# Performance work log

Hardware: AMD Instinct MI355X
Metric: run time of the kernel (lower is better)

The kernel has to match this reference:

```python
import jax, jax.numpy as jnp
import numpy as np

NPOINT = 1024
RADIUS = 0.2
NSAMPLE = 32


def fps(xyz, npoint):
    """Furthest point sampling. xyz: (B, N, 3) -> idx (B, npoint) int32.
    Sequential farthest-distance selection, first point is index 0 (matches CUDA kernel)."""
    def one(pts):
        N = pts.shape[0]
        def step(carry, _):
            dists, last = carry
            d = jnp.sum((pts - pts[last]) ** 2, axis=-1)   # (N,)
            dists = jnp.minimum(dists, d)
            nxt = jnp.argmax(dists).astype(jnp.int32)
            return (dists, nxt), last
        init = (jnp.full((N,), 1e10, dtype=pts.dtype), jnp.int32(0))
        _, idx = jax.lax.scan(step, init, None, length=npoint)
        return idx
    return jax.vmap(one)(xyz)


def ball_query(xyz, new_xyz, radius, nsample):
    """For each centroid, indices of first nsample points within radius;
    slots with no hit are filled with the first hit (centroid itself is always a hit)."""
    N = xyz.shape[1]
    d2 = jnp.sum((new_xyz[:, :, None, :] - xyz[:, None, :, :]) ** 2, axis=-1)  # (B, npoint, N)
    cand = jnp.where(d2 < radius * radius, jnp.arange(N, dtype=jnp.int32), jnp.int32(N))
    neg_topk, _ = jax.lax.top_k(-cand, nsample)  # smallest nsample candidate indices
    idx = -neg_topk                               # ascending order, misses == N
    first = idx[..., :1]
    return jnp.where(idx == N, first, idx)


_batched_gather = jax.vmap(lambda a, i: a[i])  # a: (N, C), i: (...,) -> (..., C)


def reference(xyz, normal, features, w1, b1, w2, b2, w3, b3):
    # --- FPS sampling + gather of centroids ---
    fps_idx = fps(xyz, NPOINT)                          # (B, npoint)
    new_xyz = _batched_gather(xyz, fps_idx)             # (B, npoint, 3)
    new_normal = _batched_gather(normal, fps_idx)       # (B, npoint, 3)

    # --- ball-query grouping ---
    idx = ball_query(xyz, new_xyz, RADIUS, NSAMPLE)     # (B, npoint, nsample)
    grouped_xyz = _batched_gather(xyz, idx) - new_xyz[:, :, None, :]  # relative coords
    grouped_feat = _batched_gather(features, idx)        # (B, npoint, nsample, C)
    h = jnp.concatenate([grouped_xyz, grouped_feat], axis=-1)  # (B, npoint, nsample, 3+C)

    # --- shared per-neighborhood MLP (1x1 convs) + max pool over neighbors ---
    h = jax.nn.relu(jnp.einsum('bpsc,co->bpso', h, w1) + b1)
    h = jax.nn.relu(jnp.einsum('bpsc,co->bpso', h, w2) + b2)
    h = jax.nn.relu(jnp.einsum('bpsc,co->bpso', h, w3) + b3)
    new_features = jnp.max(h, axis=2)                   # (B, npoint, 128)
    new_features = jnp.transpose(new_features, (0, 2, 1))  # (B, 128, npoint) channel-first
    return new_xyz, new_normal, new_features


def setup_inputs() -> dict:
    key = jax.random.key(0)
    ks = jax.random.split(key, 9)
    B, N, C = 8, 8192, 32
    cin = 3 + C
    return {
        'xyz': jax.random.uniform(ks[0], (B, N, 3), dtype=jnp.float32),
        'normal': jax.random.normal(ks[1], (B, N, 3), dtype=jnp.float32),
        'features': jax.random.normal(ks[2], (B, N, C), dtype=jnp.float32),
        'w1': jax.random.normal(ks[3], (cin, 64), dtype=jnp.float32) * (1.0 / np.sqrt(cin)),
        'b1': jnp.zeros((64,), dtype=jnp.float32),
        'w2': jax.random.normal(ks[4], (64, 64), dtype=jnp.float32) * (1.0 / np.sqrt(64)),
        'b2': jnp.zeros((64,), dtype=jnp.float32),
        'w3': jax.random.normal(ks[5], (64, 128), dtype=jnp.float32) * (1.0 / np.sqrt(64)),
        'b3': jnp.zeros((128,), dtype=jnp.float32),
    }
```

## Files before the change

### kernel.cpp

```cpp
#include <hip/hip_runtime.h>

#define NB 8
#define NN 8192
#define NC 32
#define NPOINT 1024
#define NSAMPLE 32

__device__ __forceinline__ float d2_exact(float ax, float ay, float az,
                                          float bx, float by, float bz) {
    float dx = __fsub_rn(ax, bx);
    float dy = __fsub_rn(ay, by);
    float dz = __fsub_rn(az, bz);
    return __fadd_rn(__fadd_rn(__fmul_rn(dx, dx), __fmul_rn(dy, dy)),
                     __fmul_rn(dz, dz));
}

#define FPS_T 256
#define FPS_K (NN / FPS_T)
#define NCONS 248
#define NBLK (NB + NCONS)
#define K2_WAVES 4
#define SLOTS_PER_PASS (NCONS * K2_WAVES)
#define NPASS ((NB * NPOINT + SLOTS_PER_PASS - 1) / SLOTS_PER_PASS)

#define XS 37
#define HS 65

#define SMEM_BYTES 102464

__device__ __forceinline__ unsigned long long kmax64(unsigned long long a,
                                                     unsigned long long b) {
    double r = fmax(__longlong_as_double((long long)a),
                    __longlong_as_double((long long)b));
    return (unsigned long long)__double_as_longlong(r);
}

template <int CTRL, int RM>
__device__ __forceinline__ unsigned long long dpp_k(unsigned long long k) {
    unsigned hi = (unsigned)__builtin_amdgcn_update_dpp(
        0, (int)(k >> 32), CTRL, RM, 0xf, true);
    unsigned lo = (unsigned)__builtin_amdgcn_update_dpp(
        0, (int)(k & 0xffffffffULL), CTRL, RM, 0xf, true);
    return ((unsigned long long)hi << 32) | lo;
}

__device__ __forceinline__ void barrier_lds_only() {
    asm volatile("s_waitcnt lgkmcnt(0)\n\ts_barrier" ::: "memory");
}

__global__ __launch_bounds__(256, 1) void fused_kernel(
    const float* __restrict__ xyz, const float* __restrict__ normal,
    const float* __restrict__ features,
    const float* __restrict__ w1, const float* __restrict__ b1,
    const float* __restrict__ w2, const float* __restrict__ b2,
    const float* __restrict__ w3, const float* __restrict__ b3,
    float* __restrict__ out_xyz, float* __restrict__ out_normal,
    float* __restrict__ out_feat, int* __restrict__ idxbuf) {

    __shared__ __align__(16) char smem[SMEM_BYTES];

    if (blockIdx.x < NB) {
        unsigned long long (*redk)[4] = (unsigned long long (*)[4])(smem);
        int*   sel_hist = (int*)(smem + 64);
        float* sxyz     = (float*)(smem + 64 + 4096);

        const int b = blockIdx.x;
        const float* bx = xyz + (size_t)b * NN * 3;
        const int tid = threadIdx.x;
        const int lane = tid & 63;
        const int wave = tid >> 6;
        int* idxg = idxbuf + (b << 10);

        float px[FPS_K], py[FPS_K], pz[FPS_K], dist[FPS_K];
#pragma unroll
        for (int k = 0; k < FPS_K; ++k) {
            int p = tid + k * FPS_T;
            float x = bx[p * 3 + 0];
            float y = bx[p * 3 + 1];
            float z = bx[p * 3 + 2];
            px[k] = x; py[k] = y; pz[k] = z;
            sxyz[p * 3 + 0] = x;
            sxyz[p * 3 + 1] = y;
            sxyz[p * 3 + 2] = z;
            dist[k] = 1e10f;
        }
#pragma unroll
        for (int k = 0; k < FPS_K; ++k) {
            asm volatile("" : "+v"(px[k]), "+v"(py[k]), "+v"(pz[k]));
        }

        int cur = 0;
        float lx = bx[0], ly = bx[1], lz = bx[2];

        for (int it = 0; it < NPOINT; ++it) {
            const int par = it & 1;
            if (tid == 0) sel_hist[it] = cur;

            float bv[4] = {-1.0f, -1.0f, -1.0f, -1.0f};
            int bk[4] = {0, 0, 0, 0};
#pragma unroll
            for (int k = 0; k < FPS_K; ++k) {
                const int c = k >> 3;
                float d = d2_exact(px[k], py[k], pz[k], lx, ly, lz);
                float nd = fminf(dist[k], d);
                dist[k] = nd;
                bool gt = nd > bv[c];
                bv[c] = gt ? nd : bv[c];
                bk[c] = gt ? k : bk[c];
            }
            bool g1 = bv[1] > bv[0];
            float v01 = g1 ? bv[1] : bv[0];
            int   k01 = g1 ? bk[1] : bk[0];
            bool g3 = bv[3] > bv[2];
            float v23 = g3 ? bv[3] : bv[2];
            int   k23 = g3 ? bk[3] : bk[2];
            bool gf = v23 > v01;
            float bvf = gf ? v23 : v01;
            int   bkf = gf ? k23 : k01;

            int bp = tid + (bkf << 8);
            unsigned long long key =
                ((unsigned long long)__float_as_uint(bvf) << 32) |
                (unsigned)(~bp);

            key = kmax64(key, dpp_k<0x111, 0xf>(key));
            key = kmax64(key, dpp_k<0x112, 0xf>(key));
            key = kmax64(key, dpp_k<0x114, 0xf>(key));
            key = kmax64(key, dpp_k<0x118, 0xf>(key));
            key = kmax64(key, dpp_k<0x142, 0xa>(key));
            key = kmax64(key, dpp_k<0x143, 0xc>(key));
            if (lane == 63) redk[par][wave] = key;
            barrier_lds_only();

            unsigned long long g =
                kmax64(kmax64(redk[par][0], redk[par][1]),
                       kmax64(redk[par][2], redk[par][3]));
            int p = (int)(~(unsigned)(g & 0xffffffffULL));
            p = __builtin_amdgcn_readfirstlane(p);
            lx = sxyz[p * 3 + 0];
            ly = sxyz[p * 3 + 1];
            lz = sxyz[p * 3 + 2];
            cur = p;

            if (((it & 15) == 15) && tid < 16) {
                int t = (it & ~15) + tid;
                __hip_atomic_store(idxg + t, sel_hist[t], __ATOMIC_RELAXED,
                                   __HIP_MEMORY_SCOPE_AGENT);
            }
        }
        __syncthreads();

        const float* bn = normal + (size_t)b * NN * 3;
        for (int t = tid; t < NPOINT; t += FPS_T) {
            int i = sel_hist[t];
            size_t o = ((size_t)b * NPOINT + t) * 3;
            out_xyz[o + 0] = sxyz[i * 3 + 0];
            out_xyz[o + 1] = sxyz[i * 3 + 1];
            out_xyz[o + 2] = sxyz[i * 3 + 2];
            out_normal[o + 0] = bn[i * 3 + 0];
            out_normal[o + 1] = bn[i * 3 + 1];
            out_normal[o + 2] = bn[i * 3 + 2];
        }
    } else {
        int*   sel_all  = (int*)smem;
        float* bufA_all = (float*)(smem + 512);
        float* bufB_all = (float*)(smem + 33792);

        const int cb = blockIdx.x - NB;
        const int wave = threadIdx.x >> 6;
        const int lane = threadIdx.x & 63;
        int*   sel = sel_all + wave * 32;
        float* XA  = bufA_all + wave * 2080;
        float* XB  = bufB_all + wave * 2080;

        for (int pass = 0; pass < NPASS; ++pass) {
            int k = pass * SLOTS_PER_PASS + (cb * K2_WAVES + wave);
            if (k >= NB * NPOINT) k -= NB * NPOINT;
            const int b = k & 7;
            const int t = k >> 3;
            const int g = (b << 10) + t;
            const int p = t;
            const float* bxp = xyz + (size_t)b * NN * 3;
            const float* bfp = features + (size_t)b * NN * NC;

            int v = __hip_atomic_load(idxbuf + g, __ATOMIC_RELAXED,
                                      __HIP_MEMORY_SCOPE_AGENT);
            while (v < 0) {
                __builtin_amdgcn_s_sleep(8);
                v = __hip_atomic_load(idxbuf + g, __ATOMIC_RELAXED,
                                      __HIP_MEMORY_SCOPE_AGENT);
            }
            const float cx = bxp[v * 3 + 0];
            const float cy = bxp[v * 3 + 1];
            const float cz = bxp[v * 3 + 2];

            int have = 0;
            for (int ch = 0; ch < NN / 64 && have < NSAMPLE; ++ch) {
                int j = ch * 64 + lane;
                float x = bxp[j * 3 + 0], y = bxp[j * 3 + 1], z = bxp[j * 3 + 2];
                float d2 = d2_exact(x, y, z, cx, cy, cz);
                bool hit = d2 < 0.04f;
                unsigned long long m = __ballot(hit);
                int pos = have + __popcll(m & ((1ull << lane) - 1ull));
                if (hit && pos < NSAMPLE) sel[pos] = j;
                have += __popcll(m);
            }
            __syncthreads();
            int nsel = have < NSAMPLE ? have : NSAMPLE;
            int first = sel[0];
            if (lane < NSAMPLE && lane >= nsel) sel[lane] = first;
            __syncthreads();

            {
                int s = lane >> 1, h = lane & 1;
                int row = sel[s];
                const float* fr = bfp + (size_t)row * NC + h * 16;
#pragma unroll
                for (int q = 0; q < 4; ++q) {
                    float4 vv = *(const float4*)(fr + q * 4);
                    int base = s * XS + 3 + h * 16 + q * 4;
                    XA[base + 0] = vv.x; XA[base + 1] = vv.y;
                    XA[base + 2] = vv.z; XA[base + 3] = vv.w;
                }
                if (h == 0) {
                    XA[s * XS + 0] = __fsub_rn(bxp[row * 3 + 0], cx);
                    XA[s * XS + 1] = __fsub_rn(bxp[row * 3 + 1], cy);
                    XA[s * XS + 2] = __fsub_rn(bxp[row * 3 + 2], cz);
                }
            }
            __syncthreads();

            const int sg = lane >> 3;
            const int og = lane & 7;

            {
                float acc[4][8];
#pragma unroll
                for (int j = 0; j < 4; ++j)
#pragma unroll
                    for (int o = 0; o < 8; ++o) acc[j][o] = 0.f;
                for (int c = 0; c < 35; ++c) {
                    float xv[4];
#pragma unroll
                    for (int j = 0; j < 4; ++j) xv[j] = XA[(sg * 4 + j) * XS + c];
                    const float* wr = w1 + c * 64 + og * 8;
                    float4 wa = *(const float4*)(wr);
                    float4 wb = *(const float4*)(wr + 4);
                    float w8[8] = {wa.x, wa.y, wa.z, wa.w, wb.x, wb.y, wb.z, wb.w};
#pragma unroll
                    for (int j = 0; j < 4; ++j)
#pragma unroll
                        for (int o = 0; o < 8; ++o) acc[j][o] += xv[j] * w8[o];
                }
                float4 ba = *(const float4*)(b1 + og * 8);
                float4 bb = *(const float4*)(b1 + og * 8 + 4);
                float bias[8] = {ba.x, ba.y, ba.z, ba.w, bb.x, bb.y, bb.z, bb.w};
#pragma unroll
                for (int j = 0; j < 4; ++j)
#pragma unroll
                    for (int o = 0; o < 8; ++o)
                        XB[(sg * 4 + j) * HS + og * 8 + o] =
                            fmaxf(acc[j][o] + bias[o], 0.f);
            }
            __syncthreads();

            {
                float acc[4][8];
#pragma unroll
                for (int j = 0; j < 4; ++j)
#pragma unroll
                    for (int o = 0; o < 8; ++o) acc[j][o] = 0.f;
                for (int c = 0; c < 64; ++c) {
                    float xv[4];
#pragma unroll
                    for (int j = 0; j < 4; ++j) xv[j] = XB[(sg * 4 + j) * HS + c];
                    const float* wr = w2 + c * 64 + og * 8;
                    float4 wa = *(const float4*)(wr);
                    float4 wb = *(const float4*)(wr + 4);
                    float w8[8] = {wa.x, wa.y, wa.z, wa.w, wb.x, wb.y, wb.z, wb.w};
#pragma unroll
                    for (int j = 0; j < 4; ++j)
#pragma unroll
                        for (int o = 0; o < 8; ++o) acc[j][o] += xv[j] * w8[o];
                }
                float4 ba = *(const float4*)(b2 + og * 8);
                float4 bb = *(const float4*)(b2 + og * 8 + 4);
                float bias[8] = {ba.x, ba.y, ba.z, ba.w, bb.x, bb.y, bb.z, bb.w};
#pragma unroll
                for (int j = 0; j < 4; ++j)
#pragma unroll
                    for (int o = 0; o < 8; ++o)
                        XA[(sg * 4 + j) * HS + og * 8 + o] =
                            fmaxf(acc[j][o] + bias[o], 0.f);
            }
            __syncthreads();

            {
                float acc[4][16];
#pragma unroll
                for (int j = 0; j < 4; ++j)
#pragma unroll
                    for (int o = 0; o < 16; ++o) acc[j][o] = 0.f;
                for (int c = 0; c < 64; ++c) {
                    float xv[4];
#pragma unroll
                    for (int j = 0; j < 4; ++j) xv[j] = XA[(sg * 4 + j) * HS + c];
                    const float* wr = w3 + c * 128 + og * 16;
                    float4 wq[4];
#pragma unroll
                    for (int q = 0; q < 4; ++q) wq[q] = *(const float4*)(wr + q * 4);
                    float w16[16] = {wq[0].x, wq[0].y, wq[0].z, wq[0].w,
                                     wq[1].x, wq[1].y, wq[1].z, wq[1].w,
                                     wq[2].x, wq[2].y, wq[2].z, wq[2].w,
                                     wq[3].x, wq[3].y, wq[3].z, wq[3].w};
#pragma unroll
                    for (int j = 0; j < 4; ++j)
#pragma unroll
                        for (int o = 0; o < 16; ++o) acc[j][o] += xv[j] * w16[o];
                }
                float m[16];
#pragma unroll
                for (int o = 0; o < 16; ++o) {
                    float t0 = fmaxf(acc[0][o], acc[1][o]);
                    float t1 = fmaxf(acc[2][o], acc[3][o]);
                    m[o] = fmaxf(t0, t1);
                }
#pragma unroll
                for (int off = 8; off <= 32; off <<= 1)
#pragma unroll
                    for (int o = 0; o < 16; ++o)
                        m[o] = fmaxf(m[o], __shfl_xor(m[o], off));
                if (sg == 0) {
                    float4 bq[4];
#pragma unroll
                    for (int q = 0; q < 4; ++q)
                        bq[q] = *(const float4*)(b3 + og * 16 + q * 4);
                    float bias[16] = {bq[0].x, bq[0].y, bq[0].z, bq[0].w,
                                      bq[1].x, bq[1].y, bq[1].z, bq[1].w,
                                      bq[2].x, bq[2].y, bq[2].z, bq[2].w,
                                      bq[3].x, bq[3].y, bq[3].z, bq[3].w};
#pragma unroll
                    for (int o = 0; o < 16; ++o) {
                        float val = fmaxf(m[o] + bias[o], 0.f);
                        out_feat[((size_t)b * 128 + og * 16 + o) * NPOINT + p] = val;
                    }
                }
            }
        }
    }
}

extern "C" void kernel_launch(void* const* d_in, const int* in_sizes, int n_in,
                              void* d_out, int out_size, void* d_ws, size_t ws_size,
                              hipStream_t stream) {
    const float* xyz      = (const float*)d_in[0];
    const float* normal   = (const float*)d_in[1];
    const float* features = (const float*)d_in[2];
    const float* w1 = (const float*)d_in[3];
    const float* b1 = (const float*)d_in[4];
    const float* w2 = (const float*)d_in[5];
    const float* b2 = (const float*)d_in[6];
    const float* w3 = (const float*)d_in[7];
    const float* b3 = (const float*)d_in[8];

    float* out        = (float*)d_out;
    float* out_xyz    = out;
    float* out_normal = out + NB * NPOINT * 3;
    float* out_feat   = out + 2 * NB * NPOINT * 3;
    int*   idxbuf     = (int*)d_ws;

    hipMemsetAsync(idxbuf, 0xFF, NB * NPOINT * sizeof(int), stream);

    hipLaunchKernelGGL(fused_kernel, dim3(NBLK), dim3(256), 0, stream,
                       xyz, normal, features, w1, b1, w2, b2, w3, b3,
                       out_xyz, out_normal, out_feat, idxbuf);
}
```

Baseline: 1.025 ms.

## Pack FPS distance math into v_pk ops and split wave argmax reduction

Stores the FPS point coordinates as float2 pairs and computes the squared distances with packed v_pk_add/v_pk_mul instructions, halving the VALU instruction count for the distance update. The 64-bit key DPP reduction is replaced by a float max reduction, a readlane, and then an unsigned min reduction over the indices of lanes holding the max, so the ties rule stays the same. Selected indices are now published to global memory one per iteration by thread 0 rather than in batches of 16, so consumer blocks see them earlier at the cost of a global store each iteration. Packed add of the negated centroid plus separate mul and add should match the original rounding, though this depends on v_pk ops not fusing.

After: 1.127 ms. 10.0% more time.

```diff
diff --git a/kernel.cpp b/kernel.cpp
--- a/kernel.cpp
+++ b/kernel.cpp
@@ -28,6 +28,19 @@
 
 #define SMEM_BYTES 102464
 
+typedef float f32x2 __attribute__((ext_vector_type(2)));
+
+__device__ __forceinline__ f32x2 pk_add(f32x2 a, f32x2 b) {
+    f32x2 d;
+    asm("v_pk_add_f32 %0, %1, %2" : "=v"(d) : "v"(a), "v"(b));
+    return d;
+}
+__device__ __forceinline__ f32x2 pk_mul(f32x2 a, f32x2 b) {
+    f32x2 d;
+    asm("v_pk_mul_f32 %0, %1, %2" : "=v"(d) : "v"(a), "v"(b));
+    return d;
+}
+
 __device__ __forceinline__ unsigned long long kmax64(unsigned long long a,
                                                      unsigned long long b) {
     double r = fmax(__longlong_as_double((long long)a),
@@ -36,12 +49,14 @@
 }
 
 template <int CTRL, int RM>
-__device__ __forceinline__ unsigned long long dpp_k(unsigned long long k) {
-    unsigned hi = (unsigned)__builtin_amdgcn_update_dpp(
-        0, (int)(k >> 32), CTRL, RM, 0xf, true);
-    unsigned lo = (unsigned)__builtin_amdgcn_update_dpp(
-        0, (int)(k & 0xffffffffULL), CTRL, RM, 0xf, true);
-    return ((unsigned long long)hi << 32) | lo;
+__device__ __forceinline__ float dpp_f(float x) {
+    return __int_as_float(__builtin_amdgcn_update_dpp(
+        0, __float_as_int(x), CTRL, RM, 0xf, true));
+}
+template <int CTRL, int RM>
+__device__ __forceinline__ unsigned dpp_u(unsigned x) {
+    return (unsigned)__builtin_amdgcn_update_dpp(
+        -1, (int)x, CTRL, RM, 0xf, false);
 }
 
 __device__ __forceinline__ void barrier_lds_only() {
@@ -71,22 +86,24 @@
         const int wave = tid >> 6;
         int* idxg = idxbuf + (b << 10);
 
-        float px[FPS_K], py[FPS_K], pz[FPS_K], dist[FPS_K];
+        f32x2 px[FPS_K / 2], py[FPS_K / 2], pz[FPS_K / 2];
+        float dist[FPS_K];
 #pragma unroll
         for (int k = 0; k < FPS_K; ++k) {
             int p = tid + k * FPS_T;
             float x = bx[p * 3 + 0];
             float y = bx[p * 3 + 1];
             float z = bx[p * 3 + 2];
-            px[k] = x; py[k] = y; pz[k] = z;
             sxyz[p * 3 + 0] = x;
             sxyz[p * 3 + 1] = y;
             sxyz[p * 3 + 2] = z;
+            if ((k & 1) == 0) { px[k >> 1].x = x; py[k >> 1].x = y; pz[k >> 1].x = z; }
+            else              { px[k >> 1].y = x; py[k >> 1].y = y; pz[k >> 1].y = z; }
             dist[k] = 1e10f;
         }
 #pragma unroll
-        for (int k = 0; k < FPS_K; ++k) {
-            asm volatile("" : "+v"(px[k]), "+v"(py[k]), "+v"(pz[k]));
+        for (int q = 0; q < FPS_K / 2; ++q) {
+            asm volatile("" : "+v"(px[q]), "+v"(py[q]), "+v"(pz[q]));
         }
 
         int cur = 0;
@@ -94,19 +111,36 @@
 
         for (int it = 0; it < NPOINT; ++it) {
             const int par = it & 1;
-            if (tid == 0) sel_hist[it] = cur;
+            if (tid == 0) {
+                sel_hist[it] = cur;
+                __hip_atomic_store(idxg + it, cur, __ATOMIC_RELAXED,
+                                   __HIP_MEMORY_SCOPE_AGENT);
+            }
+
+            f32x2 nlx = {-lx, -lx};
+            f32x2 nly = {-ly, -ly};
+            f32x2 nlz = {-lz, -lz};
 
             float bv[4] = {-1.0f, -1.0f, -1.0f, -1.0f};
             int bk[4] = {0, 0, 0, 0};
 #pragma unroll
-            for (int k = 0; k < FPS_K; ++k) {
-                const int c = k >> 3;
-                float d = d2_exact(px[k], py[k], pz[k], lx, ly, lz);
-                float nd = fminf(dist[k], d);
-                dist[k] = nd;
-                bool gt = nd > bv[c];
-                bv[c] = gt ? nd : bv[c];
-                bk[c] = gt ? k : bk[c];
+            for (int q = 0; q < FPS_K / 2; ++q) {
+                const int c = q >> 2;
+                f32x2 dx = pk_add(px[q], nlx);
+                f32x2 dy = pk_add(py[q], nly);
+                f32x2 dz = pk_add(pz[q], nlz);
+                f32x2 d2 = pk_add(pk_add(pk_mul(dx, dx), pk_mul(dy, dy)),
+                                  pk_mul(dz, dz));
+                float nd0 = fminf(dist[2 * q + 0], d2.x);
+                float nd1 = fminf(dist[2 * q + 1], d2.y);
+                dist[2 * q + 0] = nd0;
+                dist[2 * q + 1] = nd1;
+                bool g0 = nd0 > bv[c];
+                bv[c] = g0 ? nd0 : bv[c];
+                bk[c] = g0 ? 2 * q + 0 : bk[c];
+                bool g1 = nd1 > bv[c];
+                bv[c] = g1 ? nd1 : bv[c];
+                bk[c] = g1 ? 2 * q + 1 : bk[c];
             }
             bool g1 = bv[1] > bv[0];
             float v01 = g1 ? bv[1] : bv[0];
@@ -119,17 +153,31 @@
             int   bkf = gf ? k23 : k01;
 
             int bp = tid + (bkf << 8);
-            unsigned long long key =
-                ((unsigned long long)__float_as_uint(bvf) << 32) |
-                (unsigned)(~bp);
-
-            key = kmax64(key, dpp_k<0x111, 0xf>(key));
-            key = kmax64(key, dpp_k<0x112, 0xf>(key));
-            key = kmax64(key, dpp_k<0x114, 0xf>(key));
-            key = kmax64(key, dpp_k<0x118, 0xf>(key));
-            key = kmax64(key, dpp_k<0x142, 0xa>(key));
-            key = kmax64(key, dpp_k<0x143, 0xc>(key));
-            if (lane == 63) redk[par][wave] = key;
+
+            float wm = bvf;
+            wm = fmaxf(wm, dpp_f<0x111, 0xf>(wm));
+            wm = fmaxf(wm, dpp_f<0x112, 0xf>(wm));
+            wm = fmaxf(wm, dpp_f<0x114, 0xf>(wm));
+            wm = fmaxf(wm, dpp_f<0x118, 0xf>(wm));
+            wm = fmaxf(wm, dpp_f<0x142, 0xa>(wm));
+            wm = fmaxf(wm, dpp_f<0x143, 0xc>(wm));
+            float wmax = __int_as_float(
+                __builtin_amdgcn_readlane(__float_as_int(wm), 63));
+
+            unsigned cand = (bvf == wmax) ? (unsigned)bp : 0xFFFFFFFFu;
+            cand = min(cand, dpp_u<0x111, 0xf>(cand));
+            cand = min(cand, dpp_u<0x112, 0xf>(cand));
+            cand = min(cand, dpp_u<0x114, 0xf>(cand));
+            cand = min(cand, dpp_u<0x118, 0xf>(cand));
+            cand = min(cand, dpp_u<0x142, 0xa>(cand));
+            cand = min(cand, dpp_u<0x143, 0xc>(cand));
+
+            if (lane == 63) {
+                unsigned long long key =
+                    ((unsigned long long)__float_as_uint(wmax) << 32) |
+                    (unsigned)(~cand);
+                redk[par][wave] = key;
+            }
             barrier_lds_only();
 
             unsigned long long g =
@@ -141,12 +189,6 @@
             ly = sxyz[p * 3 + 1];
             lz = sxyz[p * 3 + 2];
             cur = p;
-
-            if (((it & 15) == 15) && tid < 16) {
-                int t = (it & ~15) + tid;
-                __hip_atomic_store(idxg + t, sel_hist[t], __ATOMIC_RELAXED,
-                                   __HIP_MEMORY_SCOPE_AGENT);
-            }
         }
         __syncthreads();
 
```

## Process final centroids cooperatively per block to shorten the pipeline tail

Applied to the files above, without the earlier changes.

Consumer blocks now run eight full per-wave passes and then spend a whole 256-thread block on one remaining centroid, with work split across samples and output groups. The wrap-around duplicate slots of the old ninth pass are removed. Each FPS block also processes its own last centroid right after finishing sampling, so that centroid does not wait for a consumer to notice it. The goal is to cut the serial latency after FPS completes, since the last centroids only become available at the very end. The cost is extra code, shared-memory reuse, and more block-level barriers in the tail.

New measurement: 1.026 ms. No clear change (+0.1%).

```diff
diff --git a/kernel.cpp b/kernel.cpp
--- a/kernel.cpp
+++ b/kernel.cpp
@@ -21,7 +21,8 @@
 #define NBLK (NB + NCONS)
 #define K2_WAVES 4
 #define SLOTS_PER_PASS (NCONS * K2_WAVES)
-#define NPASS ((NB * NPOINT + SLOTS_PER_PASS - 1) / SLOTS_PER_PASS)
+#define NBULK 8
+#define NFINAL (NB * NPOINT - NBULK * SLOTS_PER_PASS)
 
 #define XS 37
 #define HS 65
@@ -46,6 +47,169 @@
 
 __device__ __forceinline__ void barrier_lds_only() {
     asm volatile("s_waitcnt lgkmcnt(0)\n\ts_barrier" ::: "memory");
+}
+
+__device__ void coop_centroid(
+    int b, int t, const float* __restrict__ xyz,
+    const float* __restrict__ features,
+    const float* __restrict__ w1, const float* __restrict__ b1,
+    const float* __restrict__ w2, const float* __restrict__ b2,
+    const float* __restrict__ w3, const float* __restrict__ b3,
+    float* __restrict__ out_feat, int* __restrict__ idxbuf,
+    char* smem, int tid) {
+    const int wave = tid >> 6;
+    const int lane = tid & 63;
+    int*   sel  = (int*)smem;
+    float* A    = (float*)(smem + 512);
+    float* H1   = (float*)(smem + 33792);
+    float* pmax = (float*)(smem + 33792 + 8320);
+
+    const int g = (b << 10) + t;
+    const float* bxp = xyz + (size_t)b * NN * 3;
+    const float* bfp = features + (size_t)b * NN * NC;
+
+    int v = __hip_atomic_load(idxbuf + g, __ATOMIC_RELAXED,
+                              __HIP_MEMORY_SCOPE_AGENT);
+    while (v < 0) {
+        __builtin_amdgcn_s_sleep(8);
+        v = __hip_atomic_load(idxbuf + g, __ATOMIC_RELAXED,
+                              __HIP_MEMORY_SCOPE_AGENT);
+    }
+    const float cx = bxp[v * 3 + 0];
+    const float cy = bxp[v * 3 + 1];
+    const float cz = bxp[v * 3 + 2];
+
+    if (wave == 0) {
+        int have = 0;
+        for (int ch = 0; ch < NN / 64 && have < NSAMPLE; ++ch) {
+            int j = ch * 64 + lane;
+            float x = bxp[j * 3 + 0], y = bxp[j * 3 + 1], z = bxp[j * 3 + 2];
+            float d2 = d2_exact(x, y, z, cx, cy, cz);
+            bool hit = d2 < 0.04f;
+            unsigned long long m = __ballot(hit);
+            int pos = have + __popcll(m & ((1ull << lane) - 1ull));
+            if (hit && pos < NSAMPLE) sel[pos] = j;
+            have += __popcll(m);
+        }
+        int nsel = have < NSAMPLE ? have : NSAMPLE;
+        int first = sel[0];
+        if (lane < NSAMPLE && lane >= nsel) sel[lane] = first;
+    }
+    __syncthreads();
+
+    {
+        int s = tid >> 3, h = tid & 7;
+        int row = sel[s];
+        float4 v4 = *(const float4*)(bfp + (size_t)row * NC + h * 4);
+        int base = s * XS + 3 + h * 4;
+        A[base + 0] = v4.x; A[base + 1] = v4.y;
+        A[base + 2] = v4.z; A[base + 3] = v4.w;
+        if (h == 0) {
+            A[s * XS + 0] = __fsub_rn(bxp[row * 3 + 0], cx);
+            A[s * XS + 1] = __fsub_rn(bxp[row * 3 + 1], cy);
+            A[s * XS + 2] = __fsub_rn(bxp[row * 3 + 2], cz);
+        }
+    }
+    __syncthreads();
+
+    const int sample = tid >> 3;
+    const int og = tid & 7;
+
+    {
+        float acc[8];
+#pragma unroll
+        for (int o = 0; o < 8; ++o) acc[o] = 0.f;
+        for (int c = 0; c < 35; ++c) {
+            float xv = A[sample * XS + c];
+            const float* wr = w1 + c * 64 + og * 8;
+            float4 wa = *(const float4*)(wr);
+            float4 wb = *(const float4*)(wr + 4);
+            float w8[8] = {wa.x, wa.y, wa.z, wa.w, wb.x, wb.y, wb.z, wb.w};
+#pragma unroll
+            for (int o = 0; o < 8; ++o) acc[o] += xv * w8[o];
+        }
+        float4 ba = *(const float4*)(b1 + og * 8);
+        float4 bb = *(const float4*)(b1 + og * 8 + 4);
+        float bias[8] = {ba.x, ba.y, ba.z, ba.w, bb.x, bb.y, bb.z, bb.w};
+#pragma unroll
+        for (int o = 0; o < 8; ++o)
+            H1[sample * HS + og * 8 + o] = fmaxf(acc[o] + bias[o], 0.f);
+    }
+    __syncthreads();
+
+    {
+        float acc[8];
+#pragma unroll
+        for (int o = 0; o < 8; ++o) acc[o] = 0.f;
+        for (int c = 0; c < 64; ++c) {
+            float xv = H1[sample * HS + c];
+            const float* wr = w2 + c * 64 + og * 8;
+            float4 wa = *(const float4*)(wr);
+            float4 wb = *(const float4*)(wr + 4);
+            float w8[8] = {wa.x, wa.y, wa.z, wa.w, wb.x, wb.y, wb.z, wb.w};
+#pragma unroll
+            for (int o = 0; o < 8; ++o) acc[o] += xv * w8[o];
+        }
+        float4 ba = *(const float4*)(b2 + og * 8);
+        float4 bb = *(const float4*)(b2 + og * 8 + 4);
+        float bias[8] = {ba.x, ba.y, ba.z, ba.w, bb.x, bb.y, bb.z, bb.w};
+#pragma unroll
+        for (int o = 0; o < 8; ++o)
+            A[sample * HS + og * 8 + o] = fmaxf(acc[o] + bias[o], 0.f);
+    }
+    __syncthreads();
+
+    {
+        float acc[16];
+#pragma unroll
+        for (int o = 0; o < 16; ++o) acc[o] = 0.f;
+        for (int c = 0; c < 64; ++c) {
+            float xv = A[sample * HS + c];
+            const float* wr = w3 + c * 128 + og * 16;
+            float4 wq[4];
+#pragma unroll
+            for (int q = 0; q < 4; ++q) wq[q] = *(const float4*)(wr + q * 4);
+            float w16[16] = {wq[0].x, wq[0].y, wq[0].z, wq[0].w,
+                             wq[1].x, wq[1].y, wq[1].z, wq[1].w,
+                             wq[2].x, wq[2].y, wq[2].z, wq[2].w,
+                             wq[3].x, wq[3].y, wq[3].z, wq[3].w};
+#pragma unroll
+            for (int o = 0; o < 16; ++o) acc[o] += xv * w16[o];
+        }
+        float m[16];
+#pragma unroll
+        for (int o = 0; o < 16; ++o) m[o] = acc[o];
+#pragma unroll
+        for (int off = 8; off <= 32; off <<= 1)
+#pragma unroll
+            for (int o = 0; o < 16; ++o) m[o] = fmaxf(m[o], __shfl_xor(m[o], off));
+        if (lane < 8) {
+#pragma unroll
+            for (int o = 0; o < 16; ++o)
+                pmax[wave * 128 + (lane & 7) * 16 + o] = m[o];
+        }
+    }
+    __syncthreads();
+
+    if (tid < 8) {
+        int oo = tid;
+        float4 bq[4];
+#pragma unroll
+        for (int q = 0; q < 4; ++q) bq[q] = *(const float4*)(b3 + oo * 16 + q * 4);
+        float bias[16] = {bq[0].x, bq[0].y, bq[0].z, bq[0].w,
+                          bq[1].x, bq[1].y, bq[1].z, bq[1].w,
+                          bq[2].x, bq[2].y, bq[2].z, bq[2].w,
+                          bq[3].x, bq[3].y, bq[3].z, bq[3].w};
+#pragma unroll
+        for (int o = 0; o < 16; ++o) {
+            float mv = fmaxf(fmaxf(pmax[0 * 128 + oo * 16 + o],
+                                   pmax[1 * 128 + oo * 16 + o]),
+                             fmaxf(pmax[2 * 128 + oo * 16 + o],
+                                   pmax[3 * 128 + oo * 16 + o]));
+            float val = fmaxf(mv + bias[o], 0.f);
+            out_feat[((size_t)b * 128 + oo * 16 + o) * NPOINT + t] = val;
+        }
+    }
 }
 
 __global__ __launch_bounds__(256, 1) void fused_kernel(
@@ -161,6 +325,10 @@
             out_normal[o + 1] = bn[i * 3 + 1];
             out_normal[o + 2] = bn[i * 3 + 2];
         }
+        __syncthreads();
+
+        coop_centroid(b, NPOINT - 1, xyz, features, w1, b1, w2, b2, w3, b3,
+                      out_feat, idxbuf, smem, tid);
     } else {
         int*   sel_all  = (int*)smem;
         float* bufA_all = (float*)(smem + 512);
@@ -173,9 +341,8 @@
         float* XA  = bufA_all + wave * 2080;
         float* XB  = bufB_all + wave * 2080;
 
-        for (int pass = 0; pass < NPASS; ++pass) {
+        for (int pass = 0; pass < NBULK; ++pass) {
             int k = pass * SLOTS_PER_PASS + (cb * K2_WAVES + wave);
-            if (k >= NB * NPOINT) k -= NB * NPOINT;
             const int b = k & 7;
             const int t = k >> 3;
             const int g = (b << 10) + t;
@@ -346,6 +513,13 @@
                     }
                 }
             }
+        }
+        __syncthreads();
+
+        {
+            int k2 = NBULK * SLOTS_PER_PASS + cb;
+            coop_centroid(k2 & 7, k2 >> 3, xyz, features, w1, b1, w2, b2,
+                          w3, b3, out_feat, idxbuf, smem, threadIdx.x);
         }
     }
 }
```
